# Optimization experiments

Measured on AMD Instinct MI355X. Metric: run time of the kernel, lower is better.

## Reference

```python
import jax, jax.numpy as jnp
import numpy as np

N, E = 10000, 320000
D, H, C = 256, 8, 32   # dim, heads, head_dim (dim//num_head)
DE, DF = 64, 1024      # edge_dim, dim_ff


def setup_inputs() -> dict:
    key = jax.random.key(0)
    ks = jax.random.split(key, 32)
    s = 0.05
    n = lambda k, shp: jax.random.normal(k, shp, jnp.float32) * s
    inp = {
        "nf": jax.random.normal(ks[0], (N, D), jnp.float32),
        "ei": jax.random.randint(ks[1], (2, E), 0, N),
        "ew": jax.random.normal(ks[2], (E, DE), jnp.float32),
        # GATConv 1
        "lin1": n(ks[3], (D, H * C)), "le1": n(ks[4], (DE, H * C)),
        "asrc1": n(ks[5], (H, C)), "adst1": n(ks[6], (H, C)), "aedge1": n(ks[7], (H, C)),
        "b1": jnp.zeros((H * C,), jnp.float32),
        # GATConv 2
        "lin2": n(ks[8], (D, H * C)), "le2": n(ks[9], (DE, H * C)),
        "asrc2": n(ks[10], (H, C)), "adst2": n(ks[11], (H, C)), "aedge2": n(ks[12], (H, C)),
        "b2": jnp.zeros((H * C,), jnp.float32),
        # LayerNorms
        "g1": jnp.ones((D,), jnp.float32), "be1": jnp.zeros((D,), jnp.float32),
        "g2": jnp.ones((D,), jnp.float32), "be2": jnp.zeros((D,), jnp.float32),
        "g3": jnp.ones((D,), jnp.float32), "be3": jnp.zeros((D,), jnp.float32),
        # FFN
        "w1": n(ks[13], (D, DF)), "fb1": jnp.zeros((DF,), jnp.float32),
        "w2": n(ks[14], (DF, D)), "fb2": jnp.zeros((D,), jnp.float32),
    }
    return inp


def _ln(x, g, b, eps=1e-6):
    # annotated-transformer LayerNorm: unbiased std, eps added to std
    mu = x.mean(-1, keepdims=True)
    sd = jnp.std(x, axis=-1, ddof=1, keepdims=True)
    return g * (x - mu) / (sd + eps) + b


def _gat(x, src, dst, ea, W, We, a_s, a_d, a_e, bias):
    # PyG GATConv with edge_dim, add_self_loops=True, fill_value='mean', concat=True
    ones = jnp.ones((src.shape[0], 1), x.dtype)
    cnt = jax.ops.segment_sum(ones, dst, num_segments=N)
    loop_attr = jax.ops.segment_sum(ea, dst, num_segments=N) / jnp.maximum(cnt, 1.0)
    idx = jnp.arange(N)
    srcf = jnp.concatenate([src, idx])
    dstf = jnp.concatenate([dst, idx])
    eaf = jnp.concatenate([ea, loop_attr], axis=0)          # [E+N, DE]
    xs = (x @ W).reshape(N, H, C)                            # [N,H,C]
    ef = (eaf @ We).reshape(-1, H, C)                        # [E+N,H,C]
    a_src = (xs * a_s).sum(-1)                               # [N,H]
    a_dst = (xs * a_d).sum(-1)                               # [N,H]
    alpha = a_src[srcf] + a_dst[dstf] + (ef * a_e).sum(-1)   # [E+N,H]
    alpha = jax.nn.leaky_relu(alpha, 0.2)
    m = jax.ops.segment_max(alpha, dstf, num_segments=N)     # segment softmax
    ex = jnp.exp(alpha - m[dstf])
    den = jax.ops.segment_sum(ex, dstf, num_segments=N)
    w = ex / (den[dstf] + 1e-16)                             # [E+N,H]
    out = jax.ops.segment_sum(w[:, :, None] * xs[srcf], dstf, num_segments=N)
    return out.reshape(N, H * C) + bias


def reference(nf, ei, ew, lin1, le1, asrc1, adst1, aedge1, b1,
              lin2, le2, asrc2, adst2, aedge2, b2,
              g1, be1, g2, be2, g3, be3, w1, fb1, w2, fb2):
    src, dst = ei[0], ei[1]
    h = _gat(nf, src, dst, ew, lin1, le1, asrc1, adst1, aedge1, b1)
    nf = nf + jax.nn.leaky_relu(_ln(h, g1, be1), 0.01)
    h = _gat(nf, src, dst, ew, lin2, le2, asrc2, adst2, aedge2, b2)
    nf = nf + jax.nn.leaky_relu(_ln(h, g2, be2), 0.01)
    h = jax.nn.relu(nf @ w1 + fb1) @ w2 + fb2
    nf = nf + jax.nn.leaky_relu(_ln(h, g3, be3), 0.01)
    return nf
```

## Files before the change

### kernel.cpp

```cpp
#include <hip/hip_runtime.h>
#include <hip/hip_bf16.h>
#include <math.h>

#define D 256
#define H 8
#define C 32
#define DE 64
#define DF 1024

static inline size_t align_up(size_t x, size_t a) { return (x + a - 1) / a * a; }

typedef __attribute__((ext_vector_type(8))) short short8;
typedef __attribute__((ext_vector_type(4))) float f32x4;

__device__ inline unsigned short f2b(float x) {
    __hip_bfloat16 h = __float2bfloat16(x);
    return *reinterpret_cast<unsigned short*>(&h);
}
__device__ inline float b2f(unsigned short u) {
    return __uint_as_float(((unsigned int)u) << 16);
}

__global__ void deg_kernel(const int* __restrict__ dst, int* __restrict__ deg, int E) {
    int e = blockIdx.x * 256 + threadIdx.x;
    if (e < E) atomicAdd(&deg[dst[e]], 1);
}

__global__ void partial_sum_kernel(const int* __restrict__ deg, int* __restrict__ part, int n) {
    int i = blockIdx.x * 256 + threadIdx.x;
    int v = (i < n) ? deg[i] : 0;
    for (int o = 1; o < 64; o <<= 1) v += __shfl_xor(v, o);
    __shared__ int w4[4];
    if ((threadIdx.x & 63) == 0) w4[threadIdx.x >> 6] = v;
    __syncthreads();
    if (threadIdx.x == 0) part[blockIdx.x] = w4[0] + w4[1] + w4[2] + w4[3];
}

__global__ void scan_part_kernel(int* __restrict__ part, int nb) {
    __shared__ int buf[256];
    int t = threadIdx.x;
    buf[t] = (t < nb) ? part[t] : 0;
    __syncthreads();
    for (int s = 1; s < 256; s <<= 1) {
        int v = (t >= s) ? buf[t - s] : 0;
        __syncthreads();
        buf[t] += v;
        __syncthreads();
    }
    int excl = (t == 0) ? 0 : buf[t - 1];
    if (t < nb) part[t] = excl;
}

__global__ void scan_final_kernel(const int* __restrict__ deg, const int* __restrict__ part,
                                  int* __restrict__ off, int* __restrict__ cursor, int n) {
    int b = blockIdx.x, t = threadIdx.x, i = b * 256 + t;
    __shared__ int buf[256];
    int v = (i < n) ? deg[i] : 0;
    buf[t] = v;
    __syncthreads();
    for (int s = 1; s < 256; s <<= 1) {
        int x = (t >= s) ? buf[t - s] : 0;
        __syncthreads();
        buf[t] += x;
        __syncthreads();
    }
    int excl = part[b] + buf[t] - v;
    if (i < n) { off[i] = excl; cursor[i] = excl; }
    if (i == n - 1) off[n] = excl + v;
}

__global__ void fill_kernel(const int* __restrict__ src, const int* __restrict__ dst,
                            int* __restrict__ cursor, int* __restrict__ eid,
                            int* __restrict__ src_csr, int E) {
    int e = blockIdx.x * 256 + threadIdx.x;
    if (e < E) {
        int p = atomicAdd(&cursor[dst[e]], 1);
        eid[p] = e;
        src_csr[p] = src[e];
    }
}

__global__ void prep_kernel(const float* __restrict__ lin1, const float* __restrict__ lin2,
                            const float* __restrict__ w1, const float* __restrict__ w2,
                            const float* __restrict__ le1, const float* __restrict__ ae1,
                            const float* __restrict__ le2, const float* __restrict__ ae2,
                            const float* __restrict__ nf0,
                            unsigned short* __restrict__ lin1T, unsigned short* __restrict__ lin2T,
                            unsigned short* __restrict__ w1T, unsigned short* __restrict__ w2T,
                            unsigned short* __restrict__ MeT, unsigned short* __restrict__ Abf,
                            size_t n_valid, size_t n_total) {
    int b = blockIdx.x;
    if (b > 640) {
        size_t i = ((size_t)(b - 641) * 256 + threadIdx.x) * 8;
        if (i >= n_total) return;
        ushort4 o0, o1;
        if (i < n_valid) {
            float4 a = *(const float4*)&nf0[i];
            float4 bb = *(const float4*)&nf0[i + 4];
            o0.x = f2b(a.x); o0.y = f2b(a.y); o0.z = f2b(a.z); o0.w = f2b(a.w);
            o1.x = f2b(bb.x); o1.y = f2b(bb.y); o1.z = f2b(bb.z); o1.w = f2b(bb.w);
        } else {
            o0.x = o0.y = o0.z = o0.w = 0;
            o1 = o0;
        }
        *(ushort4*)&Abf[i] = o0;
        *(ushort4*)&Abf[i + 4] = o1;
        return;
    }
    if (b == 640) {
        for (int t = threadIdx.x; t < 512; t += 256) {
            int d = t >> 3, h = t & 7;
            float s1 = 0.f, s2 = 0.f;
            for (int c = 0; c < C; ++c) {
                s1 += le1[d * (H * C) + h * C + c] * ae1[h * C + c];
                s2 += le2[d * (H * C) + h * C + c] * ae2[h * C + c];
            }
            MeT[h * 64 + d] = f2b(s1);
            MeT[(8 + h) * 64 + d] = f2b(s2);
        }
        return;
    }
    __shared__ float tile[32][33];
    const float* in; unsigned short* outp; int K, N, tt;
    if (b < 64)       { in = lin1; outp = lin1T; K = D;  N = D;  tt = b; }
    else if (b < 128) { in = lin2; outp = lin2T; K = D;  N = D;  tt = b - 64; }
    else if (b < 384) { in = w1;   outp = w1T;   K = D;  N = DF; tt = b - 128; }
    else              { in = w2;   outp = w2T;   K = DF; N = D;  tt = b - 384; }
    int ntn = N >> 5;
    int bn = (tt % ntn) * 32, bk = (tt / ntn) * 32;
    int tx = threadIdx.x & 31, ty = threadIdx.x >> 5;
    for (int i = ty; i < 32; i += 8)
        tile[i][tx] = in[(size_t)(bk + i) * N + bn + tx];
    __syncthreads();
    for (int i = ty; i < 32; i += 8)
        outp[(size_t)(bn + i) * K + bk + tx] = f2b(tile[tx][i]);
}

template<int BM>
__global__ __launch_bounds__(256) void mfma_gemm_kernel(
    const unsigned short* __restrict__ A, const unsigned short* __restrict__ BT,
    const float* __restrict__ bias, float* __restrict__ Cf, unsigned short* __restrict__ Cb,
    int M, int Nc, int K, int relu,
    const float* __restrict__ a_s, const float* __restrict__ a_d,
    float* __restrict__ asrcO, float* __restrict__ adstO) {
    constexpr int NR = (BM == 128) ? 4 : 2;
    constexpr int AI = BM / 32;
    __shared__ unsigned short As[BM * 64];
    __shared__ unsigned short Bs[128 * 64];
    int t = threadIdx.x;
    int lane = t & 63, w = t >> 6;
    int gm0 = blockIdx.x * BM, gn0 = blockIdx.y * 128;
    f32x4 acc[4][NR] = {};
    int srow = lane >> 3, scol = (lane & 7) * 8;
    int wm = (BM == 128) ? (w >> 1) * 64 : 0;
    int wn = (BM == 128) ? (w & 1) * 64 : w * 32;
    int fr = lane & 15, fk = (lane >> 4) * 8;

    for (int k0 = 0; k0 < K; k0 += 64) {
        __syncthreads();
#pragma unroll
        for (int i = 0; i < AI; ++i) {
            int rb = w * (8 * AI) + i * 8;
            const unsigned short* ga = A + (size_t)(gm0 + rb + srow) * K + k0 + scol;
            __builtin_amdgcn_global_load_lds(
                (const __attribute__((address_space(1))) unsigned int*)ga,
                (__attribute__((address_space(3))) unsigned int*)&As[rb * 64], 16, 0, 0);
        }
#pragma unroll
        for (int i = 0; i < 4; ++i) {
            int rb = w * 32 + i * 8;
            const unsigned short* gb = BT + (size_t)(gn0 + rb + srow) * K + k0 + scol;
            __builtin_amdgcn_global_load_lds(
                (const __attribute__((address_space(1))) unsigned int*)gb,
                (__attribute__((address_space(3))) unsigned int*)&Bs[rb * 64], 16, 0, 0);
        }
        __syncthreads();
#pragma unroll
        for (int kk = 0; kk < 64; kk += 32) {
            short8 a[4], b[NR];
#pragma unroll
            for (int m = 0; m < 4; ++m)
                a[m] = *(const short8*)&As[(wm + m * 16 + fr) * 64 + kk + fk];
#pragma unroll
            for (int n = 0; n < NR; ++n)
                b[n] = *(const short8*)&Bs[(wn + n * 16 + fr) * 64 + kk + fk];
#pragma unroll
            for (int m = 0; m < 4; ++m)
#pragma unroll
                for (int n = 0; n < NR; ++n)
                    acc[m][n] = __builtin_amdgcn_mfma_f32_16x16x32_bf16(a[m], b[n], acc[m][n], 0, 0, 0);
        }
    }
    int fcol = lane & 15, frow4 = (lane >> 4) * 4;
#pragma unroll
    for (int m = 0; m < 4; ++m) {
#pragma unroll
        for (int i = 0; i < 4; ++i) {
            int gr = gm0 + wm + m * 16 + frow4 + i;
            if (gr >= M) continue;
#pragma unroll
            for (int n = 0; n < NR; ++n) {
                int gc = gn0 + wn + n * 16 + fcol;
                float v = acc[m][n][i];
                if (bias) v += bias[gc];
                if (relu) v = fmaxf(v, 0.f);
                if (Cb) Cb[(size_t)gr * Nc + gc] = f2b(v);
                else    Cf[(size_t)gr * Nc + gc] = v;
            }
        }
    }
    if (BM == 64 && a_s) {
        int head = (gn0 >> 5) + w;
        float as0 = a_s[head * 32 + fcol], as1 = a_s[head * 32 + 16 + fcol];
        float ad0 = a_d[head * 32 + fcol], ad1 = a_d[head * 32 + 16 + fcol];
#pragma unroll
        for (int m = 0; m < 4; ++m) {
#pragma unroll
            for (int i = 0; i < 4; ++i) {
                float vs = acc[m][0][i] * as0 + acc[m][1][i] * as1;
                float vd = acc[m][0][i] * ad0 + acc[m][1][i] * ad1;
#pragma unroll
                for (int o = 1; o < 16; o <<= 1) {
                    vs += __shfl_xor(vs, o);
                    vd += __shfl_xor(vd, o);
                }
                int r = gm0 + m * 16 + frow4 + i;
                if (fcol == 0 && r < M) {
                    asrcO[r * 8 + head] = vs;
                    adstO[r * 8 + head] = vd;
                }
            }
        }
    }
}

__global__ __launch_bounds__(256) void ffn2_ln_kernel(
    const unsigned short* __restrict__ A, const unsigned short* __restrict__ BT,
    const float* __restrict__ bias, const float* __restrict__ nf_in,
    const float* __restrict__ gamma, const float* __restrict__ beta,
    float* __restrict__ out, int M) {
    __shared__ unsigned short As[64 * 64];
    __shared__ unsigned short Bs[256 * 64];
    __shared__ float redS1[4][64], redS2[4][64];
    __shared__ float muS[64], invS[64];
    int t = threadIdx.x, lane = t & 63, w = t >> 6;
    int gm0 = blockIdx.x * 64;
    f32x4 acc[4][4] = {};
    int srow = lane >> 3, scol = (lane & 7) * 8;
    int wn = w * 64;
    int fr = lane & 15, fk = (lane >> 4) * 8;
    for (int k0 = 0; k0 < DF; k0 += 64) {
        __syncthreads();
#pragma unroll
        for (int i = 0; i < 2; ++i) {
            int rb = w * 16 + i * 8;
            const unsigned short* ga = A + (size_t)(gm0 + rb + srow) * DF + k0 + scol;
            __builtin_amdgcn_global_load_lds(
                (const __attribute__((address_space(1))) unsigned int*)ga,
                (__attribute__((address_space(3))) unsigned int*)&As[rb * 64], 16, 0, 0);
        }
#pragma unroll
        for (int i = 0; i < 8; ++i) {
            int rb = w * 64 + i * 8;
            const unsigned short* gb = BT + (size_t)(rb + srow) * DF + k0 + scol;
            __builtin_amdgcn_global_load_lds(
                (const __attribute__((address_space(1))) unsigned int*)gb,
                (__attribute__((address_space(3))) unsigned int*)&Bs[rb * 64], 16, 0, 0);
        }
        __syncthreads();
#pragma unroll
        for (int kk = 0; kk < 64; kk += 32) {
            short8 a[4], b[4];
#pragma unroll
            for (int m = 0; m < 4; ++m)
                a[m] = *(const short8*)&As[(m * 16 + fr) * 64 + kk + fk];
#pragma unroll
            for (int n = 0; n < 4; ++n)
                b[n] = *(const short8*)&Bs[(wn + n * 16 + fr) * 64 + kk + fk];
#pragma unroll
            for (int m = 0; m < 4; ++m)
#pragma unroll
                for (int n = 0; n < 4; ++n)
                    acc[m][n] = __builtin_amdgcn_mfma_f32_16x16x32_bf16(a[m], b[n], acc[m][n], 0, 0, 0);
        }
    }
    int fcol = lane & 15, frow4 = (lane >> 4) * 4;
#pragma unroll
    for (int m = 0; m < 4; ++m) {
#pragma unroll
        for (int i = 0; i < 4; ++i) {
            float vs1 = 0.f, vs2 = 0.f;
#pragma unroll
            for (int n = 0; n < 4; ++n) {
                float vv = acc[m][n][i] + bias[wn + n * 16 + fcol];
                acc[m][n][i] = vv;
                vs1 += vv; vs2 += vv * vv;
            }
#pragma unroll
            for (int o = 1; o < 16; o <<= 1) {
                vs1 += __shfl_xor(vs1, o);
                vs2 += __shfl_xor(vs2, o);
            }
            if (fcol == 0) {
                redS1[w][m * 16 + frow4 + i] = vs1;
                redS2[w][m * 16 + frow4 + i] = vs2;
            }
        }
    }
    __syncthreads();
    if (t < 64) {
        float s1 = redS1[0][t] + redS1[1][t] + redS1[2][t] + redS1[3][t];
        float s2 = redS2[0][t] + redS2[1][t] + redS2[2][t] + redS2[3][t];
        float mu = s1 / 256.f;
        float var = fmaxf((s2 - 256.f * mu * mu) / 255.f, 0.f);
        muS[t] = mu;
        invS[t] = 1.f / (sqrtf(var) + 1e-6f);
    }
    __syncthreads();
#pragma unroll
    for (int m = 0; m < 4; ++m) {
#pragma unroll
        for (int i = 0; i < 4; ++i) {
            int r = m * 16 + frow4 + i;
            int gr = gm0 + r;
            if (gr >= M) continue;
            float mu = muS[r], inv = invS[r];
#pragma unroll
            for (int n = 0; n < 4; ++n) {
                int gc = wn + n * 16 + fcol;
                float y = gamma[gc] * (acc[m][n][i] - mu) * inv + beta[gc];
                y = y > 0.f ? y : 0.01f * y;
                out[(size_t)gr * D + gc] = nf_in[(size_t)gr * D + gc] + y;
            }
        }
    }
}

__global__ __launch_bounds__(256) void ealpha_mfma_kernel(
    const float* __restrict__ ew, const int* __restrict__ eid,
    const unsigned short* __restrict__ MeT,
    float* __restrict__ eA1c, float* __restrict__ eA2c, int E) {
    int t = threadIdx.x;
    int lane = t & 63, w = t >> 6;
    int p0 = blockIdx.x * 64 + w * 16;
    int r = lane & 15, g = lane >> 4;
    int pr = p0 + r; if (pr > E - 1) pr = E - 1;
    int er = eid[pr];
    const float* rowp = ew + (size_t)er * DE;
    float4 x0 = *(const float4*)&rowp[g * 8];
    float4 x1 = *(const float4*)&rowp[g * 8 + 4];
    float4 y0 = *(const float4*)&rowp[32 + g * 8];
    float4 y1 = *(const float4*)&rowp[32 + g * 8 + 4];
    short8 a0, a1;
    a0[0] = (short)f2b(x0.x); a0[1] = (short)f2b(x0.y); a0[2] = (short)f2b(x0.z); a0[3] = (short)f2b(x0.w);
    a0[4] = (short)f2b(x1.x); a0[5] = (short)f2b(x1.y); a0[6] = (short)f2b(x1.z); a0[7] = (short)f2b(x1.w);
    a1[0] = (short)f2b(y0.x); a1[1] = (short)f2b(y0.y); a1[2] = (short)f2b(y0.z); a1[3] = (short)f2b(y0.w);
    a1[4] = (short)f2b(y1.x); a1[5] = (short)f2b(y1.y); a1[6] = (short)f2b(y1.z); a1[7] = (short)f2b(y1.w);
    short8 b0 = *(const short8*)&MeT[r * 64 + g * 8];
    short8 b1 = *(const short8*)&MeT[r * 64 + 32 + g * 8];
    f32x4 acc = {};
    acc = __builtin_amdgcn_mfma_f32_16x16x32_bf16(a0, b0, acc, 0, 0, 0);
    acc = __builtin_amdgcn_mfma_f32_16x16x32_bf16(a1, b1, acc, 0, 0, 0);
#pragma unroll
    for (int i = 0; i < 4; ++i) {
        int p = p0 + g * 4 + i;
        if (p < E) {
            if (r < 8) eA1c[(size_t)p * 8 + r] = acc[i];
            else       eA2c[(size_t)p * 8 + (r - 8)] = acc[i];
        }
    }
}

__global__ __launch_bounds__(256) void gat_node_kernel(
    const int* __restrict__ off, const int* __restrict__ src_csr,
    const float* __restrict__ eAc,
    const float* __restrict__ asrc, const float* __restrict__ adst,
    const unsigned short* __restrict__ xsb, const float* __restrict__ nf_in,
    const float* __restrict__ bias, const float* __restrict__ gamma,
    const float* __restrict__ beta, float* __restrict__ nf_out,
    unsigned short* __restrict__ nf_out_b, int N) {
    int lane = threadIdx.x & 63;
    int n = blockIdx.x * 4 + (threadIdx.x >> 6);
    if (n >= N) return;
    int e0 = off[n], e1 = off[n + 1], deg = e1 - e0;
    int h = lane & 7;
    int hw = lane >> 3;

    float adstn = adst[n * 8 + h];
    float asn = asrc[n * 8 + h];

    float acc0 = 0.f, acc1 = 0.f, acc2 = 0.f, acc3 = 0.f;
    float den0 = 0.f, easum = 0.f;
    int nb8 = (deg + 7) >> 3;

    bool act = hw < deg;
    int sp = e0 + hw;
    int s_cur = act ? src_csr[sp] : n;
    float ea_cur = act ? eAc[(size_t)sp * 8 + h] : 0.f;
    float as_cur = act ? asrc[s_cur * 8 + h] : 0.f;

    for (int it = 0; it < nb8; ++it) {
        int base = it * 8;
        int lim = deg - base; if (lim > 8) lim = 8;

        if (lim == 8) {
            int sk[8];
#pragma unroll
            for (int kk = 0; kk < 8; ++kk) sk[kk] = __shfl(s_cur, kk * 8 + hw);
            ushort4 u[8];
#pragma unroll
            for (int kk = 0; kk < 8; ++kk)
                u[kk] = *(const ushort4*)&xsb[(size_t)sk[kk] * D + lane * 4];
            bool actn = (base + 8 + hw) < deg;
            int spn = e0 + base + 8 + hw;
            int s_nx = actn ? src_csr[spn] : n;
            float ea_nx = actn ? eAc[(size_t)spn * 8 + h] : 0.f;
            float as_nx = actn ? asrc[s_nx * 8 + h] : 0.f;
            float al = as_cur + adstn + ea_cur;
            al = al > 0.f ? al : 0.2f * al;
            float ex = act ? expf(al) : 0.f;
            den0 += ex;
            easum += ea_cur;
            float exk[8];
#pragma unroll
            for (int kk = 0; kk < 8; ++kk) exk[kk] = __shfl(ex, kk * 8 + hw);
#pragma unroll
            for (int kk = 0; kk < 8; ++kk) {
                acc0 = fmaf(exk[kk], b2f(u[kk].x), acc0);
                acc1 = fmaf(exk[kk], b2f(u[kk].y), acc1);
                acc2 = fmaf(exk[kk], b2f(u[kk].z), acc2);
                acc3 = fmaf(exk[kk], b2f(u[kk].w), acc3);
            }
            s_cur = s_nx; ea_cur = ea_nx; as_cur = as_nx; act = actn;
        } else {
            float al = as_cur + adstn + ea_cur;
            al = al > 0.f ? al : 0.2f * al;
            float ex = act ? expf(al) : 0.f;
            den0 += ex;
            easum += ea_cur;
            for (int kk = 0; kk < lim; ++kk) {
                int sl = kk * 8 + hw;
                float exk = __shfl(ex, sl);
                int skk = __shfl(s_cur, sl);
                ushort4 u = *(const ushort4*)&xsb[(size_t)skk * D + lane * 4];
                acc0 = fmaf(exk, b2f(u.x), acc0);
                acc1 = fmaf(exk, b2f(u.y), acc1);
                acc2 = fmaf(exk, b2f(u.z), acc2);
                acc3 = fmaf(exk, b2f(u.w), acc3);
            }
            act = false;
        }
    }
    den0  += __shfl_xor(den0, 8);
    den0  += __shfl_xor(den0, 16);
    den0  += __shfl_xor(den0, 32);
    easum += __shfl_xor(easum, 8);
    easum += __shfl_xor(easum, 16);
    easum += __shfl_xor(easum, 32);
    float sa = easum / (float)(deg > 0 ? deg : 1);
    float als = asn + adstn + sa;
    als = als > 0.f ? als : 0.2f * als;
    float exSelf = expf(als);
    {
        float exs = __shfl(exSelf, hw);
        ushort4 u = *(const ushort4*)&xsb[(size_t)n * D + lane * 4];
        acc0 = fmaf(exs, b2f(u.x), acc0);
        acc1 = fmaf(exs, b2f(u.y), acc1);
        acc2 = fmaf(exs, b2f(u.z), acc2);
        acc3 = fmaf(exs, b2f(u.w), acc3);
    }
    den0 += exSelf;
    float denOwn = __shfl(den0, hw);
    float inv = 1.f / (denOwn + 1e-16f);

    int t0 = lane * 4;
    float4 bi = *(const float4*)&bias[t0];
    float o0 = acc0 * inv + bi.x;
    float o1 = acc1 * inv + bi.y;
    float o2 = acc2 * inv + bi.z;
    float o3 = acc3 * inv + bi.w;

    float s1 = o0 + o1 + o2 + o3;
    float s2 = o0 * o0 + o1 * o1 + o2 * o2 + o3 * o3;
    for (int o = 1; o < 64; o <<= 1) { s1 += __shfl_xor(s1, o); s2 += __shfl_xor(s2, o); }
    float mu = s1 / 256.f;
    float var = fmaxf((s2 - 256.f * mu * mu) / 255.f, 0.f);
    float sdv = sqrtf(var) + 1e-6f;
    float4 ga = *(const float4*)&gamma[t0];
    float4 be = *(const float4*)&beta[t0];
    float4 nin = *(const float4*)&nf_in[(size_t)n * D + t0];
    float y0 = ga.x * (o0 - mu) / sdv + be.x; y0 = y0 > 0.f ? y0 : 0.01f * y0;
    float y1 = ga.y * (o1 - mu) / sdv + be.y; y1 = y1 > 0.f ? y1 : 0.01f * y1;
    float y2 = ga.z * (o2 - mu) / sdv + be.z; y2 = y2 > 0.f ? y2 : 0.01f * y2;
    float y3 = ga.w * (o3 - mu) / sdv + be.w; y3 = y3 > 0.f ? y3 : 0.01f * y3;
    float r0 = nin.x + y0, r1 = nin.y + y1, r2 = nin.z + y2, r3 = nin.w + y3;
    float4 outv; outv.x = r0; outv.y = r1; outv.z = r2; outv.w = r3;
    *(float4*)&nf_out[(size_t)n * D + t0] = outv;
    ushort4 ob; ob.x = f2b(r0); ob.y = f2b(r1); ob.z = f2b(r2); ob.w = f2b(r3);
    *(ushort4*)&nf_out_b[(size_t)n * D + t0] = ob;
}

extern "C" void kernel_launch(void* const* d_in, const int* in_sizes, int n_in,
                              void* d_out, int out_size, void* d_ws, size_t ws_size,
                              hipStream_t stream) {
    const float* nf0    = (const float*)d_in[0];
    const int*   ei     = (const int*)d_in[1];
    const float* ew     = (const float*)d_in[2];
    const float* lin1   = (const float*)d_in[3];
    const float* le1    = (const float*)d_in[4];
    const float* asrc1w = (const float*)d_in[5];
    const float* adst1w = (const float*)d_in[6];
    const float* aedge1 = (const float*)d_in[7];
    const float* b1     = (const float*)d_in[8];
    const float* lin2   = (const float*)d_in[9];
    const float* le2    = (const float*)d_in[10];
    const float* asrc2w = (const float*)d_in[11];
    const float* adst2w = (const float*)d_in[12];
    const float* aedge2 = (const float*)d_in[13];
    const float* b2     = (const float*)d_in[14];
    const float* g1     = (const float*)d_in[15];
    const float* be1    = (const float*)d_in[16];
    const float* g2     = (const float*)d_in[17];
    const float* be2    = (const float*)d_in[18];
    const float* g3     = (const float*)d_in[19];
    const float* be3    = (const float*)d_in[20];
    const float* w1     = (const float*)d_in[21];
    const float* fb1    = (const float*)d_in[22];
    const float* w2     = (const float*)d_in[23];
    const float* fb2    = (const float*)d_in[24];

    const int N = in_sizes[0] / D;
    const int E = in_sizes[1] / 2;
    const int Mpad = ((N + 127) / 128) * 128;
    const int* srcI = ei;
    const int* dstI = ei + E;

    char* ws = (char*)d_ws;
    size_t ob = 0;
    auto alloc = [&](size_t bytes) { void* p = ws + ob; ob = align_up(ob + bytes, 256); return p; };
    int*   deg     = (int*)alloc((size_t)N * 4);
    int*   csr_off = (int*)alloc((size_t)(N + 1) * 4);
    int*   cursor  = (int*)alloc((size_t)N * 4);
    int*   part    = (int*)alloc(1024);
    int*   eid     = (int*)alloc((size_t)E * 4);
    int*   src_csr = (int*)alloc((size_t)E * 4);
    unsigned short* MeT = (unsigned short*)alloc(16 * 64 * 2);
    float* asrcB   = (float*)alloc((size_t)N * H * 4);
    float* adstB   = (float*)alloc((size_t)N * H * 4);
    float* eA1c    = (float*)alloc((size_t)E * H * 4);
    float* eA2c    = (float*)alloc((size_t)E * H * 4);
    float* nfw     = (float*)alloc((size_t)N * D * 4);
    unsigned short* xs_b  = (unsigned short*)alloc((size_t)Mpad * D * 2);
    unsigned short* Abf   = (unsigned short*)alloc((size_t)Mpad * D * 2);
    unsigned short* lin1T = (unsigned short*)alloc((size_t)D * D * 2);
    unsigned short* lin2T = (unsigned short*)alloc((size_t)D * D * 2);
    unsigned short* w1T   = (unsigned short*)alloc((size_t)DF * D * 2);
    unsigned short* w2T   = (unsigned short*)alloc((size_t)D * DF * 2);
    unsigned short* hidden = (unsigned short*)ws;
    (void)ws_size;
    float* out = (float*)d_out;

    hipMemsetAsync(deg, 0, (size_t)N * 4, stream);

    int eb = (E + 255) / 256;
    int nb = (N + 255) / 256;
    deg_kernel<<<eb, 256, 0, stream>>>(dstI, deg, E);
    partial_sum_kernel<<<nb, 256, 0, stream>>>(deg, part, N);
    scan_part_kernel<<<1, 256, 0, stream>>>(part, nb);
    scan_final_kernel<<<nb, 256, 0, stream>>>(deg, part, csr_off, cursor, N);
    fill_kernel<<<eb, 256, 0, stream>>>(srcI, dstI, cursor, eid, src_csr, E);

    const size_t nvalid = (size_t)N * D, ntot = (size_t)Mpad * D;
    int cb = (int)((ntot / 8 + 255) / 256);
    prep_kernel<<<641 + cb, 256, 0, stream>>>(lin1, lin2, w1, w2, le1, aedge1, le2, aedge2, nf0,
                                              lin1T, lin2T, w1T, w2T, MeT, Abf, nvalid, ntot);
    ealpha_mfma_kernel<<<(E + 63) / 64, 256, 0, stream>>>(ew, eid, MeT, eA1c, eA2c, E);

    int gatb = (N + 3) / 4;

    mfma_gemm_kernel<64><<<dim3(Mpad / 64, 2), 256, 0, stream>>>(
        Abf, lin1T, nullptr, nullptr, xs_b, N, D, D, 0, asrc1w, adst1w, asrcB, adstB);
    gat_node_kernel<<<gatb, 256, 0, stream>>>(csr_off, src_csr, eA1c, asrcB, adstB,
                                              xs_b, nf0, b1, g1, be1, nfw, Abf, N);
    mfma_gemm_kernel<64><<<dim3(Mpad / 64, 2), 256, 0, stream>>>(
        Abf, lin2T, nullptr, nullptr, xs_b, N, D, D, 0, asrc2w, adst2w, asrcB, adstB);
    gat_node_kernel<<<gatb, 256, 0, stream>>>(csr_off, src_csr, eA2c, asrcB, adstB,
                                              xs_b, nfw, b2, g2, be2, nfw, Abf, N);
    mfma_gemm_kernel<128><<<dim3(Mpad / 128, 8), 256, 0, stream>>>(
        Abf, w1T, fb1, nullptr, hidden, Mpad, DF, D, 1, nullptr, nullptr, nullptr, nullptr);
    ffn2_ln_kernel<<<(N + 63) / 64, 256, 0, stream>>>(hidden, w2T, fb2, nfw, g3, be3, out, N);
}
```

Baseline: 239.0 us.

## Double-buffer neighbor feature gathers in GAT aggregation with deeper index prefetch

Restructures the per-node edge aggregation loop into a software pipeline with two register buffers (uA/uB): the bf16 feature rows for the next batch of 8 edges are gathered while the current batch is accumulated. Source indices and edge attention terms are prefetched three batches ahead. The goal is to hide gather latency in this memory-bound aggregation. The cost is much higher register pressure, which may lower occupancy. The partial-batch tail is now handled through predicated lanes instead of a separate loop.

```diff
diff --git a/kernel.cpp b/kernel.cpp
--- a/kernel.cpp
+++ b/kernel.cpp
@@ -393,64 +393,83 @@
     float den0 = 0.f, easum = 0.f;
     int nb8 = (deg + 7) >> 3;
 
-    bool act = hw < deg;
-    int sp = e0 + hw;
-    int s_cur = act ? src_csr[sp] : n;
-    float ea_cur = act ? eAc[(size_t)sp * 8 + h] : 0.f;
-    float as_cur = act ? asrc[s_cur * 8 + h] : 0.f;
-
-    for (int it = 0; it < nb8; ++it) {
-        int base = it * 8;
-        int lim = deg - base; if (lim > 8) lim = 8;
-
-        if (lim == 8) {
-            int sk[8];
-#pragma unroll
-            for (int kk = 0; kk < 8; ++kk) sk[kk] = __shfl(s_cur, kk * 8 + hw);
-            ushort4 u[8];
-#pragma unroll
-            for (int kk = 0; kk < 8; ++kk)
-                u[kk] = *(const ushort4*)&xsb[(size_t)sk[kk] * D + lane * 4];
-            bool actn = (base + 8 + hw) < deg;
-            int spn = e0 + base + 8 + hw;
-            int s_nx = actn ? src_csr[spn] : n;
-            float ea_nx = actn ? eAc[(size_t)spn * 8 + h] : 0.f;
-            float as_nx = actn ? asrc[s_nx * 8 + h] : 0.f;
-            float al = as_cur + adstn + ea_cur;
-            al = al > 0.f ? al : 0.2f * al;
-            float ex = act ? expf(al) : 0.f;
-            den0 += ex;
-            easum += ea_cur;
-            float exk[8];
-#pragma unroll
-            for (int kk = 0; kk < 8; ++kk) exk[kk] = __shfl(ex, kk * 8 + hw);
-#pragma unroll
-            for (int kk = 0; kk < 8; ++kk) {
-                acc0 = fmaf(exk[kk], b2f(u[kk].x), acc0);
-                acc1 = fmaf(exk[kk], b2f(u[kk].y), acc1);
-                acc2 = fmaf(exk[kk], b2f(u[kk].z), acc2);
-                acc3 = fmaf(exk[kk], b2f(u[kk].w), acc3);
-            }
-            s_cur = s_nx; ea_cur = ea_nx; as_cur = as_nx; act = actn;
-        } else {
-            float al = as_cur + adstn + ea_cur;
-            al = al > 0.f ? al : 0.2f * al;
-            float ex = act ? expf(al) : 0.f;
-            den0 += ex;
-            easum += ea_cur;
-            for (int kk = 0; kk < lim; ++kk) {
-                int sl = kk * 8 + hw;
-                float exk = __shfl(ex, sl);
-                int skk = __shfl(s_cur, sl);
-                ushort4 u = *(const ushort4*)&xsb[(size_t)skk * D + lane * 4];
-                acc0 = fmaf(exk, b2f(u.x), acc0);
-                acc1 = fmaf(exk, b2f(u.y), acc1);
-                acc2 = fmaf(exk, b2f(u.z), acc2);
-                acc3 = fmaf(exk, b2f(u.w), acc3);
-            }
-            act = false;
-        }
-    }
+#define LOAD_SE(b, S, EA, A) { A = ((b) * 8 + hw) < deg; int sp_ = e0 + (b) * 8 + hw; \
+    S = A ? src_csr[sp_] : n; EA = A ? eAc[(size_t)sp_ * 8 + h] : 0.f; }
+
+    if (nb8 > 0) {
+        int s0, s1, s2; float ea0, ea1, ea2; bool a0, a1, a2;
+        LOAD_SE(0, s0, ea0, a0);
+        LOAD_SE(1, s1, ea1, a1);
+        LOAD_SE(2, s2, ea2, a2);
+        float as0 = a0 ? asrc[s0 * 8 + h] : 0.f;
+        float as1 = a1 ? asrc[s1 * 8 + h] : 0.f;
+        ushort4 uA[8], uB[8];
+#pragma unroll
+        for (int kk = 0; kk < 8; ++kk) {
+            int sk = __shfl(s0, kk * 8 + hw);
+            uA[kk] = *(const ushort4*)&xsb[(size_t)sk * D + lane * 4];
+        }
+        int it = 0;
+        while (true) {
+            if (it + 1 < nb8) {
+#pragma unroll
+                for (int kk = 0; kk < 8; ++kk) {
+                    int sk = __shfl(s1, kk * 8 + hw);
+                    uB[kk] = *(const ushort4*)&xsb[(size_t)sk * D + lane * 4];
+                }
+            }
+            {
+                float as2 = a2 ? asrc[s2 * 8 + h] : 0.f;
+                int s3; float ea3; bool a3;
+                LOAD_SE(it + 3, s3, ea3, a3);
+                float al = as0 + adstn + ea0;
+                al = al > 0.f ? al : 0.2f * al;
+                float ex = a0 ? expf(al) : 0.f;
+                den0 += ex; easum += ea0;
+#pragma unroll
+                for (int kk = 0; kk < 8; ++kk) {
+                    float exk = __shfl(ex, kk * 8 + hw);
+                    acc0 = fmaf(exk, b2f(uA[kk].x), acc0);
+                    acc1 = fmaf(exk, b2f(uA[kk].y), acc1);
+                    acc2 = fmaf(exk, b2f(uA[kk].z), acc2);
+                    acc3 = fmaf(exk, b2f(uA[kk].w), acc3);
+                }
+                s0 = s1; ea0 = ea1; as0 = as1; a0 = a1;
+                s1 = s2; ea1 = ea2; as1 = as2; a1 = a2;
+                s2 = s3; ea2 = ea3; a2 = a3;
+            }
+            if (++it >= nb8) break;
+            if (it + 1 < nb8) {
+#pragma unroll
+                for (int kk = 0; kk < 8; ++kk) {
+                    int sk = __shfl(s1, kk * 8 + hw);
+                    uA[kk] = *(const ushort4*)&xsb[(size_t)sk * D + lane * 4];
+                }
+            }
+            {
+                float as2 = a2 ? asrc[s2 * 8 + h] : 0.f;
+                int s3; float ea3; bool a3;
+                LOAD_SE(it + 3, s3, ea3, a3);
+                float al = as0 + adstn + ea0;
+                al = al > 0.f ? al : 0.2f * al;
+                float ex = a0 ? expf(al) : 0.f;
+                den0 += ex; easum += ea0;
+#pragma unroll
+                for (int kk = 0; kk < 8; ++kk) {
+                    float exk = __shfl(ex, kk * 8 + hw);
+                    acc0 = fmaf(exk, b2f(uB[kk].x), acc0);
+                    acc1 = fmaf(exk, b2f(uB[kk].y), acc1);
+                    acc2 = fmaf(exk, b2f(uB[kk].z), acc2);
+                    acc3 = fmaf(exk, b2f(uB[kk].w), acc3);
+                }
+                s0 = s1; ea0 = ea1; as0 = as1; a0 = a1;
+                s1 = s2; ea1 = ea2; as1 = as2; a1 = a2;
+                s2 = s3; ea2 = ea3; a2 = a3;
+            }
+            if (++it >= nb8) break;
+        }
+    }
+#undef LOAD_SE
     den0  += __shfl_xor(den0, 8);
     den0  += __shfl_xor(den0, 16);
     den0  += __shfl_xor(den0, 32);
@@ -480,11 +499,11 @@
     float o2 = acc2 * inv + bi.z;
     float o3 = acc3 * inv + bi.w;
 
-    float s1 = o0 + o1 + o2 + o3;
-    float s2 = o0 * o0 + o1 * o1 + o2 * o2 + o3 * o3;
-    for (int o = 1; o < 64; o <<= 1) { s1 += __shfl_xor(s1, o); s2 += __shfl_xor(s2, o); }
-    float mu = s1 / 256.f;
-    float var = fmaxf((s2 - 256.f * mu * mu) / 255.f, 0.f);
+    float s1r = o0 + o1 + o2 + o3;
+    float s2r = o0 * o0 + o1 * o1 + o2 * o2 + o3 * o3;
+    for (int o = 1; o < 64; o <<= 1) { s1r += __shfl_xor(s1r, o); s2r += __shfl_xor(s2r, o); }
+    float mu = s1r / 256.f;
+    float var = fmaxf((s2r - 256.f * mu * mu) / 255.f, 0.f);
     float sdv = sqrtf(var) + 1e-6f;
     float4 ga = *(const float4*)&gamma[t0];
     float4 be = *(const float4*)&beta[t0];
```

Measured after the change: 238.4 us. Within noise of the previous version (-0.2%).
